# Optimization experiments

Hardware: AMD Instinct MI355X
Metric: run time of the kernel (lower is better)

Reference implementation:

```python
import jax, jax.numpy as jnp
import numpy as np

N_MET = 250_000
N_RXN = 500_000
E_SUB = 2_000_000
E_ALL = 4_000_000
HIDDEN = 64
MSG_DIM = 32
DT = 0.01  # flux-limiting step size (forward called with dt > 0)


def setup_inputs() -> dict:
    key = jax.random.key(0)
    ks = jax.random.split(key, 12)
    inp = {}
    inp["x"] = jax.random.uniform(ks[0], (N_MET, 8), dtype=jnp.float32)
    inp["met_sub"] = jax.random.randint(ks[1], (E_SUB,), 0, N_MET, dtype=jnp.int32)
    inp["rxn_sub"] = jax.random.randint(ks[2], (E_SUB,), 0, N_RXN, dtype=jnp.int32)
    inp["sto_sub"] = jax.random.uniform(ks[3], (E_SUB,), dtype=jnp.float32) + 0.5  # |s_ij| > 0
    inp["met_all"] = jax.random.randint(ks[4], (E_ALL,), 0, N_MET, dtype=jnp.int32)
    inp["rxn_all"] = jax.random.randint(ks[5], (E_ALL,), 0, N_RXN, dtype=jnp.int32)
    inp["sto_all"] = jax.random.normal(ks[6], (E_ALL,), dtype=jnp.float32)
    sc = lambda fan_in: 1.0 / np.sqrt(fan_in)
    inp["W1"] = jax.random.normal(ks[7], (2, HIDDEN), dtype=jnp.float32) * sc(2)
    inp["b1"] = jnp.zeros((HIDDEN,), jnp.float32)
    inp["W2"] = jax.random.normal(ks[8], (HIDDEN, MSG_DIM), dtype=jnp.float32) * sc(HIDDEN)
    inp["b2"] = jnp.zeros((MSG_DIM,), jnp.float32)
    inp["W3"] = jax.random.normal(ks[9], (MSG_DIM, HIDDEN), dtype=jnp.float32) * sc(MSG_DIM)
    inp["b3"] = jnp.zeros((HIDDEN,), jnp.float32)
    inp["W4"] = jax.random.normal(ks[10], (HIDDEN, 1), dtype=jnp.float32) * sc(HIDDEN)
    inp["b4"] = jnp.zeros((1,), jnp.float32)
    inp["log_k"] = jax.random.uniform(ks[11], (N_RXN,), dtype=jnp.float32, minval=-3.0, maxval=-1.0)
    return inp


def reference(x, met_sub, rxn_sub, sto_sub, met_all, rxn_all, sto_all,
              W1, b1, W2, b2, W3, b3, W4, b4, log_k):
    conc = x[:, 3]                                            # [n_met]
    # per-substrate-edge message: MLP([conc_src, |s|]) -> msg_dim
    msg_in = jnp.stack([conc[met_sub], sto_sub], axis=-1)     # [E_sub, 2]
    msg = jnp.tanh(msg_in @ W1 + b1) @ W2 + b2                # [E_sub, msg_dim]
    # aggregate messages per reaction (index_add)
    h_rxn = jax.ops.segment_sum(msg, rxn_sub, num_segments=N_RXN)  # [n_rxn, msg_dim]
    # non-negative rates
    k = jnp.power(10.0, log_k)
    r = (jnp.tanh(h_rxn @ W3 + b3) @ W4 + b4)[:, 0]           # [n_rxn]
    v = k * jax.nn.softplus(r)
    # flux limiting: scale rates so no substrate is over-consumed in one dt step
    consumption = sto_sub * v[rxn_sub] * DT                   # [E_sub]
    total = jax.ops.segment_sum(consumption, met_sub, num_segments=N_MET)
    active = total > 1e-12
    met_scale = jnp.where(active,
                          jnp.minimum(conc / jnp.where(active, total, 1.0), 1.0),
                          1.0)                                # [n_met]
    edge_scale = met_scale[met_sub]
    rxn_scale = jnp.ones((N_RXN,), v.dtype).at[rxn_sub].min(edge_scale)  # amin, include_self
    v = v * rxn_scale
    # dx/dt = scatter-add of signed stoich * rate over all edges
    contrib = sto_all * v[rxn_all]                            # [E_all]
    dxdt = jax.ops.segment_sum(contrib, met_all, num_segments=N_MET)
    return dxdt[:, None]                                      # [n_met, 1]
```

## Files before the change

### kernel.cpp

```cpp
#include <hip/hip_runtime.h>

#define N_MET 250000
#define N_RXN 500000
#define E_SUB 2000000
#define E_ALL 4000000
#define DT 0.01f

#define RXN_PER_BLK 256
#define THREADS 256
#define EDGE_CAP 1536
#define TPAD 72

#define MV_RPB 64

#define BINSZ 1024
#define NBINS ((N_MET + BINSZ - 1) / BINSZ)
#define PART_EPB 4096
#define PTHREADS 512
#define KPB (PART_EPB / PTHREADS)
#define PART_NBLK ((E_ALL + PART_EPB - 1) / PART_EPB)
#define SPART_NBLK ((E_SUB + PART_EPB - 1) / PART_EPB)
#define RBINSZ 1024
#define RNBINS ((N_RXN + RBINSZ - 1) / RBINSZ)
#define RPART_NBLK ((E_SUB + PART_EPB - 1) / PART_EPB)

typedef int v4i __attribute__((ext_vector_type(4)));
typedef float v4f __attribute__((ext_vector_type(4)));
typedef short bf16x8 __attribute__((ext_vector_type(8)));
typedef float f32x4 __attribute__((ext_vector_type(4)));

#if __has_builtin(__builtin_amdgcn_exp2f)
#define EXP2F(x) __builtin_amdgcn_exp2f(x)
#else
#define EXP2F(x) exp2f(x)
#endif
#if __has_builtin(__builtin_amdgcn_rcpf)
#define RCPF(x) __builtin_amdgcn_rcpf(x)
#else
#define RCPF(x) __fdividef(1.0f, (x))
#endif

static __device__ __forceinline__ float fast_tanh(float x) {
  float e = __expf(x + x);
  return 1.0f - __fdividef(2.0f, e + 1.0f);
}

static __device__ __forceinline__ int bcast_i(int v, int lane) {
  return __builtin_amdgcn_readlane(v, lane);
}

static __device__ __forceinline__ unsigned short bf16_rn(float f) {
  unsigned u = __float_as_uint(f);
  unsigned r = u + 0x7FFFu + ((u >> 16) & 1u);
  return (unsigned short)(r >> 16);
}

__global__ __launch_bounds__(256) void k_bc3(
    const int* __restrict__ rxn_sub, const int* __restrict__ met_sub,
    const int* __restrict__ met_all,
    const float* __restrict__ x, float* __restrict__ conc,
    const float* __restrict__ W2, const float* __restrict__ W3,
    const float* __restrict__ b2,
    uint4* __restrict__ wfh, uint4* __restrict__ wfl, float* __restrict__ b2w3,
    int* __restrict__ rblk_cnt, int* __restrict__ sblk_cnt, int* __restrict__ blk_cnt) {
  __shared__ int cnt[RNBINS];
  int b = blockIdx.x, t = threadIdx.x;
  const int* keys; int nkeys, nblk, nb, bl; int* out;
  if (b < RPART_NBLK) {
    keys = rxn_sub; nkeys = E_SUB; nblk = RPART_NBLK; nb = RNBINS; out = rblk_cnt; bl = b;
    if (b < 2) {
      int tid = b * 256 + t;
      if (tid < 512) {
        int lane = tid & 63, jt = (tid >> 6) & 3, ks = tid >> 8;
        int jj = jt * 16 + (lane & 15);
        unsigned short h[8], l[8];
        #pragma unroll
        for (int q = 0; q < 8; ++q) {
          int kk = ks * 32 + (lane >> 4) * 8 + q;
          float w = 0.f;
          #pragma unroll
          for (int m = 0; m < 32; ++m) w = fmaf(W2[kk * 32 + m], W3[m * 64 + jj], w);
          h[q] = bf16_rn(w);
          float hf = __uint_as_float(((unsigned)h[q]) << 16);
          l[q] = bf16_rn(w - hf);
        }
        uint4 H, L;
        H.x = (unsigned)h[0] | ((unsigned)h[1] << 16);
        H.y = (unsigned)h[2] | ((unsigned)h[3] << 16);
        H.z = (unsigned)h[4] | ((unsigned)h[5] << 16);
        H.w = (unsigned)h[6] | ((unsigned)h[7] << 16);
        L.x = (unsigned)l[0] | ((unsigned)l[1] << 16);
        L.y = (unsigned)l[2] | ((unsigned)l[3] << 16);
        L.z = (unsigned)l[4] | ((unsigned)l[5] << 16);
        L.w = (unsigned)l[6] | ((unsigned)l[7] << 16);
        int idx = (ks * 4 + jt) * 64 + lane;
        wfh[idx] = H; wfl[idx] = L;
      }
      if (tid < 64) {
        float s = 0.f;
        #pragma unroll
        for (int m = 0; m < 32; ++m) s = fmaf(b2[m], W3[m * 64 + tid], s);
        b2w3[tid] = s;
      }
    }
  } else if (b < RPART_NBLK + SPART_NBLK) {
    keys = met_sub; nkeys = E_SUB; nblk = SPART_NBLK; nb = NBINS; out = sblk_cnt;
    bl = b - RPART_NBLK;
  } else {
    keys = met_all; nkeys = E_ALL; nblk = PART_NBLK; nb = NBINS; out = blk_cnt;
    bl = b - RPART_NBLK - SPART_NBLK;
    int m = bl * 256 + t;
    if (m < N_MET) conc[m] = __builtin_nontemporal_load(x + m * 8 + 3);
  }
  for (int i = t; i < nb; i += 256) cnt[i] = 0;
  __syncthreads();
  int base = bl * PART_EPB;
  #pragma unroll
  for (int i = 0; i < PART_EPB / 256; ++i) {
    int e = base + i * 256 + t;
    if (e < nkeys) atomicAdd(&cnt[__builtin_nontemporal_load(keys + e) >> 10], 1);
  }
  __syncthreads();
  for (int i = t; i < nb; i += 256) out[i * nblk + bl] = cnt[i];
}

static __device__ __forceinline__ void scan1_body(int* ss,
    const int* __restrict__ blk_cnt, int* __restrict__ blk_pref,
    int* __restrict__ bin_tot, int nblk, int j) {
  int t = threadIdx.x;
  int carry = 0;
  for (int c = 0; c < nblk; c += 256) {
    int idx = c + t;
    int v = (idx < nblk) ? blk_cnt[j * nblk + idx] : 0;
    ss[t] = v; __syncthreads();
    for (int d = 1; d < 256; d <<= 1) {
      int a = (t >= d) ? ss[t - d] : 0;
      __syncthreads();
      ss[t] += a;
      __syncthreads();
    }
    if (idx < nblk) blk_pref[j * nblk + idx] = carry + ss[t] - v;
    carry += ss[255];
    __syncthreads();
  }
  if (t == 0) bin_tot[j] = carry;
}

__global__ __launch_bounds__(256) void k_scan1all(
    const int* __restrict__ rblk_cnt, int* __restrict__ rblk_pref, int* __restrict__ rbin_tot,
    const int* __restrict__ sblk_cnt, int* __restrict__ sblk_pref, int* __restrict__ sbin_tot,
    const int* __restrict__ blk_cnt, int* __restrict__ blk_pref, int* __restrict__ bin_tot) {
  __shared__ int ss[256];
  int b = blockIdx.x;
  if (b < RNBINS)
    scan1_body(ss, rblk_cnt, rblk_pref, rbin_tot, RPART_NBLK, b);
  else if (b < RNBINS + NBINS)
    scan1_body(ss, sblk_cnt, sblk_pref, sbin_tot, SPART_NBLK, b - RNBINS);
  else
    scan1_body(ss, blk_cnt, blk_pref, bin_tot, PART_NBLK, b - RNBINS - NBINS);
}

__global__ __launch_bounds__(512) void k_scan2all(
    const int* __restrict__ rbin_tot, int* __restrict__ rbin_start,
    const int* __restrict__ sbin_tot, int* __restrict__ sbin_start,
    const int* __restrict__ bin_tot, int* __restrict__ bin_start) {
  __shared__ int ss[512];
  const int* tot; int* st; int n;
  if (blockIdx.x == 0)      { tot = rbin_tot; st = rbin_start; n = RNBINS; }
  else if (blockIdx.x == 1) { tot = sbin_tot; st = sbin_start; n = NBINS; }
  else                      { tot = bin_tot;  st = bin_start;  n = NBINS; }
  int t = threadIdx.x;
  int v = (t < n) ? tot[t] : 0;
  ss[t] = v; __syncthreads();
  for (int d = 1; d < 512; d <<= 1) {
    int a = (t >= d) ? ss[t - d] : 0;
    __syncthreads();
    ss[t] += a;
    __syncthreads();
  }
  if (t < n) st[t] = ss[t] - v;
}

template <int NB, bool PACK, typename MakeRec>
static __device__ __forceinline__ void part_sorted(
    const int* __restrict__ keys, int nkeys, int nblk,
    const int* __restrict__ blk_pref, const int* __restrict__ bin_start,
    int2* __restrict__ out, MakeRec make) {
  __shared__ int2 ordered[PART_EPB];
  __shared__ unsigned short binb[PACK ? 1 : PART_EPB];
  __shared__ int cnt[NB];
  __shared__ int gofs[NB];
  __shared__ int ss[PTHREADS];
  int b = blockIdx.x, t = threadIdx.x;
  for (int i = t; i < NB; i += PTHREADS) cnt[i] = 0;
  __syncthreads();
  int base = b * PART_EPB;
  int kbuf[KPB];
  #pragma unroll
  for (int i = 0; i < KPB; ++i) {
    int e = base + i * PTHREADS + t;
    kbuf[i] = (e < nkeys) ? __builtin_nontemporal_load(keys + e) : -1;
    if (kbuf[i] >= 0) atomicAdd(&cnt[kbuf[i] >> 10], 1);
  }
  __syncthreads();
  int v = (t < NB) ? cnt[t] : 0;
  ss[t] = v; __syncthreads();
  for (int d = 1; d < PTHREADS; d <<= 1) {
    int a = (t >= d) ? ss[t - d] : 0;
    __syncthreads();
    ss[t] += a;
    __syncthreads();
  }
  int nloc = ss[PTHREADS - 1];
  if (t < NB) {
    int ls = ss[t] - v;
    cnt[t] = ls;
    gofs[t] = bin_start[t] + blk_pref[t * nblk + b] - ls;
  }
  __syncthreads();
  #pragma unroll
  for (int i = 0; i < KPB; ++i) {
    int k = kbuf[i];
    if (k >= 0) {
      int e = base + i * PTHREADS + t;
      int bin = k >> 10;
      int2 rec = make(e, k);
      int pos = atomicAdd(&cnt[bin], 1);
      ordered[pos] = rec;
      if (!PACK) binb[pos] = (unsigned short)bin;
    }
  }
  __syncthreads();
  for (int i = t; i < nloc; i += PTHREADS) {
    int2 rec = ordered[i];
    int bin = PACK ? (int)(((unsigned)rec.x) >> 10) : (int)binb[i];
    out[gofs[bin] + i] = rec;
  }
}

__global__ __launch_bounds__(PTHREADS) void k_rpart(
    const int* __restrict__ rxn_sub, const int* __restrict__ met_sub,
    const float* __restrict__ sto_sub,
    const int* __restrict__ blk_pref, const int* __restrict__ bin_start,
    int2* __restrict__ bins_rxn) {
  part_sorted<RNBINS, false>(rxn_sub, E_SUB, RPART_NBLK, blk_pref, bin_start, bins_rxn,
    [=] __device__ (int e, int k) {
      int m = __builtin_nontemporal_load(met_sub + e);
      float st = __builtin_nontemporal_load(sto_sub + e);
      int2 rec; rec.x = ((k & (RBINSZ - 1)) << 18) | m; rec.y = __float_as_int(st);
      return rec;
    });
}

__global__ __launch_bounds__(PTHREADS) void k_part_sub(
    const int* __restrict__ met_sub, const int* __restrict__ rxn_sub,
    const float* __restrict__ sto_sub, const float* __restrict__ v_pre,
    const int* __restrict__ blk_pref, const int* __restrict__ bin_start,
    int2* __restrict__ bins_sub) {
  part_sorted<NBINS, true>(met_sub, E_SUB, SPART_NBLK, blk_pref, bin_start, bins_sub,
    [=] __device__ (int e, int k) {
      int r = __builtin_nontemporal_load(rxn_sub + e);
      float st = __builtin_nontemporal_load(sto_sub + e);
      float val = st * v_pre[r] * DT;
      int2 rec; rec.x = k; rec.y = __float_as_int(val);
      return rec;
    });
}

__global__ __launch_bounds__(PTHREADS) void k_part(
    const int* __restrict__ met_all, const int* __restrict__ rxn_all,
    const float* __restrict__ sto_all, const float* __restrict__ vfin,
    const int* __restrict__ blk_pref, const int* __restrict__ bin_start,
    int2* __restrict__ bins) {
  part_sorted<NBINS, true>(met_all, E_ALL, PART_NBLK, blk_pref, bin_start, bins,
    [=] __device__ (int e, int k) {
      int r = __builtin_nontemporal_load(rxn_all + e);
      float st = __builtin_nontemporal_load(sto_all + e);
      float val = st * vfin[r];
      int2 rec; rec.x = k; rec.y = __float_as_int(val);
      return rec;
    });
}

__global__ __launch_bounds__(512) void k_rbin(
    const int2* __restrict__ bins_rxn, const int* __restrict__ rbin_start,
    const int* __restrict__ rbin_tot, int2* __restrict__ edges8, int* __restrict__ off) {
  __shared__ int lcnt[RBINSZ];
  __shared__ int lcur[RBINSZ];
  __shared__ int ss[512];
  int j = blockIdx.x, t = threadIdx.x;
  int base = rbin_start[j], n = rbin_tot[j];
  for (int i = t; i < RBINSZ; i += 512) lcnt[i] = 0;
  __syncthreads();
  for (int i = t; i < n; i += 512) {
    int2 rec = bins_rxn[base + i];
    atomicAdd(&lcnt[((unsigned)rec.x) >> 18], 1);
  }
  __syncthreads();
  int s0 = lcnt[2 * t], s1 = lcnt[2 * t + 1];
  int tsum = s0 + s1;
  ss[t] = tsum; __syncthreads();
  for (int d = 1; d < 512; d <<= 1) {
    int a = (t >= d) ? ss[t - d] : 0;
    __syncthreads();
    ss[t] += a;
    __syncthreads();
  }
  int run = ss[t] - tsum;
  lcur[2 * t] = run;
  lcur[2 * t + 1] = run + s0;
  __syncthreads();
  int R0 = j * RBINSZ;
  for (int rl = t; rl < RBINSZ; rl += 512) {
    int r = R0 + rl;
    if (r < N_RXN) off[r] = base + lcur[rl];
  }
  if (j == 0 && t == 0) off[N_RXN] = E_SUB;
  __syncthreads();
  for (int i = t; i < n; i += 512) {
    int2 rec = bins_rxn[base + i];
    int pos = atomicAdd(&lcur[((unsigned)rec.x) >> 18], 1);
    int2 o; o.x = rec.x & 0x3FFFF; o.y = rec.y;
    edges8[base + pos] = o;
  }
}

static __device__ __forceinline__ float edge_rsum_lds(int o0, int o1, int estart,
                                                      const float2* ep,
                                                      float w1x, float w1y, float b1j) {
  float S0 = 0.f, S1 = 0.f;
  int c = o0 - estart;
  int cend = o1 - estart;
  if (c + 1 < cend) {
    float2 e0 = ep[c], e1 = ep[c + 1];
    c += 2;
    while (c + 1 < cend) {
      float2 n0 = ep[c], n1 = ep[c + 1];
      S0 += RCPF(EXP2F(fmaf(e0.x, w1x, fmaf(e0.y, w1y, b1j))) + 1.0f);
      S1 += RCPF(EXP2F(fmaf(e1.x, w1x, fmaf(e1.y, w1y, b1j))) + 1.0f);
      e0 = n0; e1 = n1;
      c += 2;
    }
    S0 += RCPF(EXP2F(fmaf(e0.x, w1x, fmaf(e0.y, w1y, b1j))) + 1.0f);
    S1 += RCPF(EXP2F(fmaf(e1.x, w1x, fmaf(e1.y, w1y, b1j))) + 1.0f);
  }
  if (c < cend) {
    float2 e0 = ep[c];
    S0 += RCPF(EXP2F(fmaf(e0.x, w1x, fmaf(e0.y, w1y, b1j))) + 1.0f);
  }
  return S0 + S1;
}

static __device__ __forceinline__ float edge_rsum_glob(int o0, int o1,
                                                       const int2* edges8,
                                                       const float* conc,
                                                       float w1x, float w1y, float b1j) {
  float S = 0.f;
  for (int c = o0; c < o1; ++c) {
    int2 rec = edges8[c];
    float cc = conc[rec.x];
    float t0 = fmaf(cc, w1x, fmaf(__int_as_float(rec.y), w1y, b1j));
    S += RCPF(EXP2F(t0) + 1.0f);
  }
  return S;
}

__global__ __launch_bounds__(THREADS) void k_edge_mv(
    const int* __restrict__ off, const int2* __restrict__ edges8,
    const float* __restrict__ conc,
    const float* __restrict__ W1, const float* __restrict__ b1,
    const uint4* __restrict__ wfh, const uint4* __restrict__ wfl,
    const float* __restrict__ b2w3, const float* __restrict__ b3,
    const float* __restrict__ W4, const float* __restrict__ b4,
    const float* __restrict__ log_k, float* __restrict__ v_pre) {
  __shared__ int off_s[RXN_PER_BLK + 1];
  __shared__ float2 se[EDGE_CAP];
  __shared__ __align__(16) unsigned short thi[4][16][TPAD];
  __shared__ __align__(16) unsigned short tlo[4][16][TPAD];

  int tid = threadIdx.x;
  int lane = tid & 63;
  int wv = tid >> 6;
  int R0 = blockIdx.x * RXN_PER_BLK;

  for (int i = tid; i <= RXN_PER_BLK; i += THREADS) {
    int r = R0 + i;
    off_s[i] = off[r > N_RXN ? N_RXN : r];
  }
  __syncthreads();
  int estart = off_s[0];
  int nE = off_s[RXN_PER_BLK] - estart;
  bool fits = (nE <= EDGE_CAP);
  if (fits) {
    for (int i = tid; i < nE; i += THREADS) {
      int2 rec = edges8[estart + i];
      se[i] = make_float2(conc[rec.x], __int_as_float(rec.y));
    }
  }

  const float C2 = 2.8853900817779268f;
  float w1x = W1[lane] * C2, w1y = W1[64 + lane] * C2, b1j = b1[lane] * C2;

  int rbase = R0 + wv * 64;
  int o0l = off_s[wv * 64 + lane];
  int o1l = off_s[wv * 64 + lane + 1];

  int col = lane & 15, rowg = lane >> 4;

  float w4c[4], bwc[4], b3c[4];
  #pragma unroll
  for (int jt = 0; jt < 4; ++jt) {
    int jj = jt * 16 + col;
    w4c[jt] = W4[jj]; bwc[jt] = b2w3[jj]; b3c[jt] = b3[jj];
  }
  float b40 = b4[0];

  __syncthreads();

  const uint4* wfh_v = wfh;
  const uint4* wfl_v = wfl;

  unsigned short* thw = &thi[wv][0][0];
  unsigned short* tlw = &tlo[wv][0][0];

  int o0 = bcast_i(o0l, 0);
  #pragma clang loop unroll(disable)
  for (int tt = 0; tt < 4; ++tt) {
    asm volatile("" : "+v"(wfh_v), "+v"(wfl_v));
    int rt = rbase + tt * 16;
    #pragma clang loop unroll(disable)
    for (int i = 0; i < 16; ++i) {
      int li = tt * 16 + i;
      int o1 = bcast_i(o1l, li);
      float S = fits ? edge_rsum_lds(o0, o1, estart, se, w1x, w1y, b1j)
                     : edge_rsum_glob(o0, o1, edges8, conc, w1x, w1y, b1j);
      float T = (float)(o1 - o0) - 2.0f * S;
      unsigned short hi = bf16_rn(T);
      float hf = __uint_as_float(((unsigned)hi) << 16);
      thw[i * TPAD + lane] = hi;
      tlw[i * TPAD + lane] = bf16_rn(T - hf);
      o0 = o1;
    }
    bf16x8 ah[2], al[2];
    {
      int fo = col * TPAD + rowg * 8;
      const uint4* ph = (const uint4*)thw;
      const uint4* pl = (const uint4*)tlw;
      ah[0] = __builtin_bit_cast(bf16x8, ph[fo >> 3]);
      ah[1] = __builtin_bit_cast(bf16x8, ph[(fo + 32) >> 3]);
      al[0] = __builtin_bit_cast(bf16x8, pl[fo >> 3]);
      al[1] = __builtin_bit_cast(bf16x8, pl[(fo + 32) >> 3]);
    }
    f32x4 acc[4];
    #pragma unroll
    for (int jt = 0; jt < 4; ++jt) acc[jt] = (f32x4){0.f, 0.f, 0.f, 0.f};
    #pragma unroll
    for (int jt = 0; jt < 4; ++jt) {
      #pragma unroll
      for (int ks = 0; ks < 2; ++ks) {
        int bidx = (ks * 4 + jt) * 64 + lane;
        bf16x8 bh = __builtin_bit_cast(bf16x8, wfh_v[bidx]);
        bf16x8 bl = __builtin_bit_cast(bf16x8, wfl_v[bidx]);
        acc[jt] = __builtin_amdgcn_mfma_f32_16x16x32_bf16(ah[ks], bh, acc[jt], 0, 0, 0);
        acc[jt] = __builtin_amdgcn_mfma_f32_16x16x32_bf16(ah[ks], bl, acc[jt], 0, 0, 0);
        acc[jt] = __builtin_amdgcn_mfma_f32_16x16x32_bf16(al[ks], bh, acc[jt], 0, 0, 0);
      }
    }
    float nq[4];
    #pragma unroll
    for (int q = 0; q < 4; ++q) {
      int idx = tt * 16 + rowg * 4 + q + wv * 64;
      nq[q] = (float)(off_s[idx + 1] - off_s[idx]);
    }
    #pragma unroll
    for (int q = 0; q < 4; ++q) {
      float s = 0.f;
      #pragma unroll
      for (int jt = 0; jt < 4; ++jt) {
        float u = acc[jt][q] + nq[q] * bwc[jt] + b3c[jt];
        s += fast_tanh(u) * w4c[jt];
      }
      s += __shfl_xor(s, 1, 64);
      s += __shfl_xor(s, 2, 64);
      s += __shfl_xor(s, 4, 64);
      s += __shfl_xor(s, 8, 64);
      if (col == 0) {
        int r = rt + rowg * 4 + q;
        float lk = (r < N_RXN) ? log_k[r] : 0.f;
        float racc = s + b40;
        float k10 = __expf(lk * 2.3025850929940457f);
        float sp = (racc > 15.f) ? racc : __logf(1.f + __expf(racc));
        if (r < N_RXN) v_pre[r] = k10 * sp;
      }
    }
  }
}

__global__ __launch_bounds__(512) void k_bins_sub(
    const int2* __restrict__ bins_sub, const int* __restrict__ bin_start,
    const int* __restrict__ bin_tot, const float* __restrict__ conc,
    float* __restrict__ met_scale) {
  __shared__ float acc[BINSZ];
  int j = blockIdx.x, t = threadIdx.x;
  for (int i = t; i < BINSZ; i += 512) acc[i] = 0.f;
  __syncthreads();
  int s0 = bin_start[j], n = bin_tot[j];
  for (int i = t; i < n; i += 512) {
    int2 rec = bins_sub[s0 + i];
    atomicAdd(&acc[rec.x & (BINSZ - 1)], __int_as_float(rec.y));
  }
  __syncthreads();
  int m0 = j * BINSZ;
  for (int i = t; i < BINSZ; i += 512) {
    int m = m0 + i;
    if (m < N_MET) {
      float tot = acc[i];
      met_scale[m] = (tot > 1e-12f) ? fminf(conc[m] / tot, 1.0f) : 1.0f;
    }
  }
}

__global__ __launch_bounds__(256) void k_rscale(
    const int* __restrict__ off, const int2* __restrict__ edges8,
    const float* __restrict__ met_scale, const float* __restrict__ v_pre,
    float* __restrict__ vfin) {
  __shared__ int soff[MV_RPB + 1];
  int tid = threadIdx.x, lane = tid & 63, w = tid >> 6;
  int B0 = blockIdx.x * MV_RPB;
  for (int i = tid; i <= MV_RPB; i += 256) {
    int r = B0 + i;
    soff[i] = off[r > N_RXN ? N_RXN : r];
  }
  __syncthreads();

  int rloc = w * 16 + (lane >> 2);
  int o0 = soff[rloc], o1 = soff[rloc + 1];
  float sc = 1.0f;
  for (int c = o0 + (lane & 3); c < o1; c += 4) {
    sc = fminf(sc, met_scale[edges8[c].x]);
  }
  sc = fminf(sc, __shfl_xor(sc, 1, 64));
  sc = fminf(sc, __shfl_xor(sc, 2, 64));
  if ((lane & 3) == 0) {
    int r = B0 + rloc;
    if (r < N_RXN) vfin[r] = v_pre[r] * sc;
  }
}

__global__ __launch_bounds__(512) void k_bins(const int2* __restrict__ bins,
                                              const int* __restrict__ bin_start,
                                              const int* __restrict__ bin_tot,
                                              float* __restrict__ dxdt) {
  __shared__ float acc[BINSZ];
  int j = blockIdx.x, t = threadIdx.x;
  for (int i = t; i < BINSZ; i += 512) acc[i] = 0.f;
  __syncthreads();
  int s0 = bin_start[j], n = bin_tot[j];
  for (int i = t; i < n; i += 512) {
    int2 rec = bins[s0 + i];
    atomicAdd(&acc[rec.x & (BINSZ - 1)], __int_as_float(rec.y));
  }
  __syncthreads();
  int m0 = j * BINSZ;
  for (int i = t; i < BINSZ; i += 512) {
    int m = m0 + i;
    if (m < N_MET) dxdt[m] = acc[i];
  }
}

extern "C" void kernel_launch(void* const* d_in, const int* in_sizes, int n_in,
                              void* d_out, int out_size, void* d_ws, size_t ws_size,
                              hipStream_t stream) {
  const float* x       = (const float*)d_in[0];
  const int*   met_sub = (const int*)d_in[1];
  const int*   rxn_sub = (const int*)d_in[2];
  const float* sto_sub = (const float*)d_in[3];
  const int*   met_all = (const int*)d_in[4];
  const int*   rxn_all = (const int*)d_in[5];
  const float* sto_all = (const float*)d_in[6];
  const float* W1    = (const float*)d_in[7];
  const float* b1    = (const float*)d_in[8];
  const float* W2    = (const float*)d_in[9];
  const float* b2    = (const float*)d_in[10];
  const float* W3    = (const float*)d_in[11];
  const float* b3    = (const float*)d_in[12];
  const float* W4    = (const float*)d_in[13];
  const float* b4    = (const float*)d_in[14];
  const float* log_k = (const float*)d_in[15];
  float* dxdt = (float*)d_out;

  char* ws = (char*)d_ws;
  size_t p = 0;
  auto alloc = [&](size_t bytes) -> void* {
    void* r = (void*)(ws + p);
    p += (bytes + 255) & ~(size_t)255;
    return r;
  };
  int*    off        = (int*)alloc(sizeof(int) * (N_RXN + 1));
  uint4*  wfh        = (uint4*)alloc(sizeof(uint4) * 512);
  uint4*  wfl        = (uint4*)alloc(sizeof(uint4) * 512);
  float*  b2w3       = (float*)alloc(sizeof(float) * 64);
  float*  v_pre      = (float*)alloc(sizeof(float) * N_RXN);
  float*  vfin       = (float*)alloc(sizeof(float) * N_RXN);
  float*  conc       = (float*)alloc(sizeof(float) * N_MET);
  float*  met_scale  = (float*)alloc(sizeof(float) * N_MET);
  int2*   edges8     = (int2*)alloc(sizeof(int2) * E_SUB);
  int2*   bins_rxn   = (int2*)alloc(sizeof(int2) * E_SUB);
  int2*   bins_sub   = (int2*)alloc(sizeof(int2) * E_SUB);
  int2*   bins       = (int2*)alloc(sizeof(int2) * E_ALL);
  int*    rblk_cnt   = (int*)alloc(sizeof(int) * RNBINS * RPART_NBLK);
  int*    rblk_pref  = (int*)alloc(sizeof(int) * RNBINS * RPART_NBLK);
  int*    sblk_cnt   = (int*)alloc(sizeof(int) * NBINS * SPART_NBLK);
  int*    sblk_pref  = (int*)alloc(sizeof(int) * NBINS * SPART_NBLK);
  int*    blk_cnt    = (int*)alloc(sizeof(int) * NBINS * PART_NBLK);
  int*    blk_pref   = (int*)alloc(sizeof(int) * NBINS * PART_NBLK);
  int*    rbin_tot   = (int*)alloc(sizeof(int) * 512);
  int*    rbin_start = (int*)alloc(sizeof(int) * 512);
  int*    sbin_tot   = (int*)alloc(sizeof(int) * 512);
  int*    sbin_start = (int*)alloc(sizeof(int) * 512);
  int*    bin_tot    = (int*)alloc(sizeof(int) * 512);
  int*    bin_start  = (int*)alloc(sizeof(int) * 512);
  (void)in_sizes; (void)n_in; (void)out_size; (void)ws_size;


  k_bc3<<<RPART_NBLK + SPART_NBLK + PART_NBLK, 256, 0, stream>>>(
      rxn_sub, met_sub, met_all, x, conc, W2, W3, b2, wfh, wfl, b2w3,
      rblk_cnt, sblk_cnt, blk_cnt);
  k_scan1all<<<RNBINS + NBINS + NBINS, 256, 0, stream>>>(
      rblk_cnt, rblk_pref, rbin_tot, sblk_cnt, sblk_pref, sbin_tot,
      blk_cnt, blk_pref, bin_tot);
  k_scan2all<<<3, 512, 0, stream>>>(rbin_tot, rbin_start, sbin_tot, sbin_start,
                                    bin_tot, bin_start);

  k_rpart<<<RPART_NBLK, PTHREADS, 0, stream>>>(rxn_sub, met_sub, sto_sub,
                                               rblk_pref, rbin_start, bins_rxn);
  k_rbin<<<RNBINS, 512, 0, stream>>>(bins_rxn, rbin_start, rbin_tot, edges8, off);

  k_edge_mv<<<(N_RXN + RXN_PER_BLK - 1) / RXN_PER_BLK, THREADS, 0, stream>>>(
      off, edges8, conc, W1, b1, wfh, wfl, b2w3, b3, W4, b4, log_k, v_pre);

  k_part_sub<<<SPART_NBLK, PTHREADS, 0, stream>>>(met_sub, rxn_sub, sto_sub, v_pre,
                                                  sblk_pref, sbin_start, bins_sub);
  k_bins_sub<<<NBINS, 512, 0, stream>>>(bins_sub, sbin_start, sbin_tot, conc, met_scale);

  k_rscale<<<(N_RXN + MV_RPB - 1) / MV_RPB, 256, 0, stream>>>(
      off, edges8, met_scale, v_pre, vfin);

  k_part<<<PART_NBLK, PTHREADS, 0, stream>>>(met_all, rxn_all, sto_all, vfin,
                                             blk_pref, bin_start, bins);
  k_bins<<<NBINS, 512, 0, stream>>>(bins, bin_start, bin_tot, dxdt);
}
```

Baseline: 415.4 us.

## Replace binned partition scatter for dxdt with direct global atomic adds

Removes the met_all histogram, prefix scans, partition and per-bin LDS accumulation for the final dxdt scatter. The output is now zeroed and accumulated directly with vectorized edge loads and global float atomicAdd. This avoids writing and re-reading 4M edge records and several extra kernel passes. The cost is contended random global atomics and a nondeterministic summation order.

```diff
diff --git a/kernel.cpp b/kernel.cpp
--- a/kernel.cpp
+++ b/kernel.cpp
@@ -18,7 +18,6 @@
 #define PART_EPB 4096
 #define PTHREADS 512
 #define KPB (PART_EPB / PTHREADS)
-#define PART_NBLK ((E_ALL + PART_EPB - 1) / PART_EPB)
 #define SPART_NBLK ((E_SUB + PART_EPB - 1) / PART_EPB)
 #define RBINSZ 1024
 #define RNBINS ((N_RXN + RBINSZ - 1) / RBINSZ)
@@ -57,17 +56,16 @@
 
 __global__ __launch_bounds__(256) void k_bc3(
     const int* __restrict__ rxn_sub, const int* __restrict__ met_sub,
-    const int* __restrict__ met_all,
     const float* __restrict__ x, float* __restrict__ conc,
     const float* __restrict__ W2, const float* __restrict__ W3,
     const float* __restrict__ b2,
     uint4* __restrict__ wfh, uint4* __restrict__ wfl, float* __restrict__ b2w3,
-    int* __restrict__ rblk_cnt, int* __restrict__ sblk_cnt, int* __restrict__ blk_cnt) {
+    int* __restrict__ rblk_cnt, int* __restrict__ sblk_cnt) {
   __shared__ int cnt[RNBINS];
   int b = blockIdx.x, t = threadIdx.x;
-  const int* keys; int nkeys, nblk, nb, bl; int* out;
+  const int* keys; int nblk, nb, bl; int* out;
   if (b < RPART_NBLK) {
-    keys = rxn_sub; nkeys = E_SUB; nblk = RPART_NBLK; nb = RNBINS; out = rblk_cnt; bl = b;
+    keys = rxn_sub; nblk = RPART_NBLK; nb = RNBINS; out = rblk_cnt; bl = b;
     if (b < 2) {
       int tid = b * 256 + t;
       if (tid < 512) {
@@ -103,14 +101,13 @@
         b2w3[tid] = s;
       }
     }
-  } else if (b < RPART_NBLK + SPART_NBLK) {
-    keys = met_sub; nkeys = E_SUB; nblk = SPART_NBLK; nb = NBINS; out = sblk_cnt;
+  } else {
+    keys = met_sub; nblk = SPART_NBLK; nb = NBINS; out = sblk_cnt;
     bl = b - RPART_NBLK;
-  } else {
-    keys = met_all; nkeys = E_ALL; nblk = PART_NBLK; nb = NBINS; out = blk_cnt;
-    bl = b - RPART_NBLK - SPART_NBLK;
-    int m = bl * 256 + t;
-    if (m < N_MET) conc[m] = __builtin_nontemporal_load(x + m * 8 + 3);
+    int m0 = bl * 512 + t;
+    if (m0 < N_MET) conc[m0] = __builtin_nontemporal_load(x + m0 * 8 + 3);
+    int m1 = m0 + 256;
+    if (m1 < N_MET) conc[m1] = __builtin_nontemporal_load(x + m1 * 8 + 3);
   }
   for (int i = t; i < nb; i += 256) cnt[i] = 0;
   __syncthreads();
@@ -118,7 +115,7 @@
   #pragma unroll
   for (int i = 0; i < PART_EPB / 256; ++i) {
     int e = base + i * 256 + t;
-    if (e < nkeys) atomicAdd(&cnt[__builtin_nontemporal_load(keys + e) >> 10], 1);
+    if (e < E_SUB) atomicAdd(&cnt[__builtin_nontemporal_load(keys + e) >> 10], 1);
   }
   __syncthreads();
   for (int i = t; i < nb; i += 256) out[i * nblk + bl] = cnt[i];
@@ -148,27 +145,22 @@
 
 __global__ __launch_bounds__(256) void k_scan1all(
     const int* __restrict__ rblk_cnt, int* __restrict__ rblk_pref, int* __restrict__ rbin_tot,
-    const int* __restrict__ sblk_cnt, int* __restrict__ sblk_pref, int* __restrict__ sbin_tot,
-    const int* __restrict__ blk_cnt, int* __restrict__ blk_pref, int* __restrict__ bin_tot) {
+    const int* __restrict__ sblk_cnt, int* __restrict__ sblk_pref, int* __restrict__ sbin_tot) {
   __shared__ int ss[256];
   int b = blockIdx.x;
   if (b < RNBINS)
     scan1_body(ss, rblk_cnt, rblk_pref, rbin_tot, RPART_NBLK, b);
-  else if (b < RNBINS + NBINS)
+  else
     scan1_body(ss, sblk_cnt, sblk_pref, sbin_tot, SPART_NBLK, b - RNBINS);
-  else
-    scan1_body(ss, blk_cnt, blk_pref, bin_tot, PART_NBLK, b - RNBINS - NBINS);
 }
 
 __global__ __launch_bounds__(512) void k_scan2all(
     const int* __restrict__ rbin_tot, int* __restrict__ rbin_start,
-    const int* __restrict__ sbin_tot, int* __restrict__ sbin_start,
-    const int* __restrict__ bin_tot, int* __restrict__ bin_start) {
+    const int* __restrict__ sbin_tot, int* __restrict__ sbin_start) {
   __shared__ int ss[512];
   const int* tot; int* st; int n;
-  if (blockIdx.x == 0)      { tot = rbin_tot; st = rbin_start; n = RNBINS; }
-  else if (blockIdx.x == 1) { tot = sbin_tot; st = sbin_start; n = NBINS; }
-  else                      { tot = bin_tot;  st = bin_start;  n = NBINS; }
+  if (blockIdx.x == 0) { tot = rbin_tot; st = rbin_start; n = RNBINS; }
+  else                 { tot = sbin_tot; st = sbin_start; n = NBINS; }
   int t = threadIdx.x;
   int v = (t < n) ? tot[t] : 0;
   ss[t] = v; __syncthreads();
@@ -262,21 +254,6 @@
       int r = __builtin_nontemporal_load(rxn_sub + e);
       float st = __builtin_nontemporal_load(sto_sub + e);
       float val = st * v_pre[r] * DT;
-      int2 rec; rec.x = k; rec.y = __float_as_int(val);
-      return rec;
-    });
-}
-
-__global__ __launch_bounds__(PTHREADS) void k_part(
-    const int* __restrict__ met_all, const int* __restrict__ rxn_all,
-    const float* __restrict__ sto_all, const float* __restrict__ vfin,
-    const int* __restrict__ blk_pref, const int* __restrict__ bin_start,
-    int2* __restrict__ bins) {
-  part_sorted<NBINS, true>(met_all, E_ALL, PART_NBLK, blk_pref, bin_start, bins,
-    [=] __device__ (int e, int k) {
-      int r = __builtin_nontemporal_load(rxn_all + e);
-      float st = __builtin_nontemporal_load(sto_all + e);
-      float val = st * vfin[r];
       int2 rec; rec.x = k; rec.y = __float_as_int(val);
       return rec;
     });
@@ -547,24 +524,24 @@
   }
 }
 
-__global__ __launch_bounds__(512) void k_bins(const int2* __restrict__ bins,
-                                              const int* __restrict__ bin_start,
-                                              const int* __restrict__ bin_tot,
-                                              float* __restrict__ dxdt) {
-  __shared__ float acc[BINSZ];
-  int j = blockIdx.x, t = threadIdx.x;
-  for (int i = t; i < BINSZ; i += 512) acc[i] = 0.f;
-  __syncthreads();
-  int s0 = bin_start[j], n = bin_tot[j];
-  for (int i = t; i < n; i += 512) {
-    int2 rec = bins[s0 + i];
-    atomicAdd(&acc[rec.x & (BINSZ - 1)], __int_as_float(rec.y));
-  }
-  __syncthreads();
-  int m0 = j * BINSZ;
-  for (int i = t; i < BINSZ; i += 512) {
-    int m = m0 + i;
-    if (m < N_MET) dxdt[m] = acc[i];
+__global__ __launch_bounds__(256) void k_zero(float* __restrict__ dxdt) {
+  int m = blockIdx.x * 256 + threadIdx.x;
+  if (m < N_MET) dxdt[m] = 0.f;
+}
+
+__global__ __launch_bounds__(256) void k_scat(
+    const v4i* __restrict__ met_all4, const v4i* __restrict__ rxn_all4,
+    const v4f* __restrict__ sto_all4, const float* __restrict__ vfin,
+    float* __restrict__ dxdt) {
+  int i = blockIdx.x * 256 + threadIdx.x;
+  if (i < E_ALL / 4) {
+    v4i m4 = __builtin_nontemporal_load(met_all4 + i);
+    v4i r4 = __builtin_nontemporal_load(rxn_all4 + i);
+    v4f s4 = __builtin_nontemporal_load(sto_all4 + i);
+    atomicAdd(&dxdt[m4.x], s4.x * vfin[r4.x]);
+    atomicAdd(&dxdt[m4.y], s4.y * vfin[r4.y]);
+    atomicAdd(&dxdt[m4.z], s4.z * vfin[r4.z]);
+    atomicAdd(&dxdt[m4.w], s4.w * vfin[r4.w]);
   }
 }
 
@@ -607,30 +584,24 @@
   int2*   edges8     = (int2*)alloc(sizeof(int2) * E_SUB);
   int2*   bins_rxn   = (int2*)alloc(sizeof(int2) * E_SUB);
   int2*   bins_sub   = (int2*)alloc(sizeof(int2) * E_SUB);
-  int2*   bins       = (int2*)alloc(sizeof(int2) * E_ALL);
   int*    rblk_cnt   = (int*)alloc(sizeof(int) * RNBINS * RPART_NBLK);
   int*    rblk_pref  = (int*)alloc(sizeof(int) * RNBINS * RPART_NBLK);
   int*    sblk_cnt   = (int*)alloc(sizeof(int) * NBINS * SPART_NBLK);
   int*    sblk_pref  = (int*)alloc(sizeof(int) * NBINS * SPART_NBLK);
-  int*    blk_cnt    = (int*)alloc(sizeof(int) * NBINS * PART_NBLK);
-  int*    blk_pref   = (int*)alloc(sizeof(int) * NBINS * PART_NBLK);
   int*    rbin_tot   = (int*)alloc(sizeof(int) * 512);
   int*    rbin_start = (int*)alloc(sizeof(int) * 512);
   int*    sbin_tot   = (int*)alloc(sizeof(int) * 512);
   int*    sbin_start = (int*)alloc(sizeof(int) * 512);
-  int*    bin_tot    = (int*)alloc(sizeof(int) * 512);
-  int*    bin_start  = (int*)alloc(sizeof(int) * 512);
   (void)in_sizes; (void)n_in; (void)out_size; (void)ws_size;
 
-
-  k_bc3<<<RPART_NBLK + SPART_NBLK + PART_NBLK, 256, 0, stream>>>(
-      rxn_sub, met_sub, met_all, x, conc, W2, W3, b2, wfh, wfl, b2w3,
-      rblk_cnt, sblk_cnt, blk_cnt);
-  k_scan1all<<<RNBINS + NBINS + NBINS, 256, 0, stream>>>(
-      rblk_cnt, rblk_pref, rbin_tot, sblk_cnt, sblk_pref, sbin_tot,
-      blk_cnt, blk_pref, bin_tot);
-  k_scan2all<<<3, 512, 0, stream>>>(rbin_tot, rbin_start, sbin_tot, sbin_start,
-                                    bin_tot, bin_start);
+  k_zero<<<(N_MET + 255) / 256, 256, 0, stream>>>(dxdt);
+
+  k_bc3<<<RPART_NBLK + SPART_NBLK, 256, 0, stream>>>(
+      rxn_sub, met_sub, x, conc, W2, W3, b2, wfh, wfl, b2w3,
+      rblk_cnt, sblk_cnt);
+  k_scan1all<<<RNBINS + NBINS, 256, 0, stream>>>(
+      rblk_cnt, rblk_pref, rbin_tot, sblk_cnt, sblk_pref, sbin_tot);
+  k_scan2all<<<2, 512, 0, stream>>>(rbin_tot, rbin_start, sbin_tot, sbin_start);
 
   k_rpart<<<RPART_NBLK, PTHREADS, 0, stream>>>(rxn_sub, met_sub, sto_sub,
                                                rblk_pref, rbin_start, bins_rxn);
@@ -646,7 +617,7 @@
   k_rscale<<<(N_RXN + MV_RPB - 1) / MV_RPB, 256, 0, stream>>>(
       off, edges8, met_scale, v_pre, vfin);
 
-  k_part<<<PART_NBLK, PTHREADS, 0, stream>>>(met_all, rxn_all, sto_all, vfin,
-                                             blk_pref, bin_start, bins);
-  k_bins<<<NBINS, 512, 0, stream>>>(bins, bin_start, bin_tot, dxdt);
-}
+  k_scat<<<(E_ALL / 4 + 255) / 256, 256, 0, stream>>>(
+      (const v4i*)met_all, (const v4i*)rxn_all, (const v4f*)sto_all,
+      vfin, dxdt);
+}
```

Measured after the change: 529.5 us. 27.5% more time.
